# Optimization experiments

Measured on AMD Instinct MI355X. Metric: run time of the kernel, lower is better.

The kernel has to match this reference:

```python
import jax, jax.numpy as jnp
import numpy as np

H = 8          # num query heads
KV = 1         # num kv heads
D = 256        # head_dim
HID = 2048     # hidden_size
B = 4          # sequences in prefill batch
S = 2048       # tokens per sequence
T = B * S      # total tokens
NUM_SLOTS = 16384
ROPE_THETA = 10000.0


def setup_inputs() -> dict:
    key = jax.random.key(0)
    k1, k2, k3 = jax.random.split(key, 3)
    hidden_states = jax.random.normal(k1, (T, HID), dtype=jnp.float32)
    # real rotary tables: positions 0..S-1 repeated per sequence
    pos = jnp.tile(jnp.arange(S, dtype=jnp.float32), B)              # [T]
    inv_freq = 1.0 / (ROPE_THETA ** (jnp.arange(0, D, 2, dtype=jnp.float32) / D))  # [D/2]
    ang = pos[:, None] * inv_freq[None, :]                            # [T, D/2]
    cos, sin = jnp.cos(ang), jnp.sin(ang)
    slots = jnp.arange(T, dtype=jnp.int32)                            # contiguous slot mapping
    key_cache = jnp.zeros((NUM_SLOTS, KV, D), dtype=jnp.float32)
    value_cache = jnp.zeros((NUM_SLOTS, KV, D), dtype=jnp.float32)
    w_qkv = jax.random.normal(k2, ((H + 2 * KV) * D, HID), dtype=jnp.float32) * (HID ** -0.5)
    w_o = jax.random.normal(k3, (HID, H * D), dtype=jnp.float32) * ((H * D) ** -0.5)
    return {"hidden_states": hidden_states, "cos": cos, "sin": sin, "slots": slots,
            "key_cache": key_cache, "value_cache": value_cache, "w_qkv": w_qkv, "w_o": w_o}


def _rope(x, cos, sin):
    # rotate-half convention: x:[T, h, D], cos/sin:[T, D/2]
    x1, x2 = x[..., : D // 2], x[..., D // 2 :]
    c, s = cos[:, None, :], sin[:, None, :]
    return jnp.concatenate([x1 * c - x2 * s, x2 * c + x1 * s], axis=-1)


def reference(hidden_states, cos, sin, slots, key_cache, value_cache, w_qkv, w_o):
    qkv = hidden_states @ w_qkv.T                                  # [T, (H+2KV)*D]
    q = qkv[:, : H * D].reshape(T, H, D)
    k = qkv[:, H * D : (H + KV) * D].reshape(T, KV, D)
    v = qkv[:, (H + KV) * D :].reshape(T, KV, D)
    q = _rope(q, cos, sin)
    k = _rope(k, cos, sin)
    # paged_attention.reshape_and_cache: scatter post-RoPE k and raw v into cache slots
    key_cache = key_cache.at[slots].set(k)
    value_cache = value_cache.at[slots].set(v)
    # prefill flash attention: causal, per-sequence (equal-length ragged batch)
    qb = q.reshape(B, S, H, D)
    kb = jnp.repeat(k.reshape(B, S, KV, D), H // KV, axis=2)       # GQA expand
    vb = jnp.repeat(v.reshape(B, S, KV, D), H // KV, axis=2)
    scale = D ** -0.5
    scores = jnp.einsum("bqhd,bkhd->bhqk", qb, kb) * scale          # [B,H,S,S]
    causal = jnp.tril(jnp.ones((S, S), dtype=bool))
    scores = jnp.where(causal[None, None], scores, jnp.finfo(scores.dtype).min)
    probs = jax.nn.softmax(scores, axis=-1)
    attn = jnp.einsum("bhqk,bkhd->bqhd", probs, vb).reshape(T, H * D)
    out = attn @ w_o.T                                              # [T, HID]
    return out, key_cache, value_cache
```

## Files before the change

### kernel.cpp

```cpp
#include <hip/hip_runtime.h>

#define HN 8
#define DH 256
#define HID 2048
#define BB 4
#define SS 2048
#define TT (BB*SS)
#define NQKV 2560
#define NSLOTS 16384

typedef unsigned short u16;
typedef unsigned int u32;
typedef __bf16 bf16x8 __attribute__((ext_vector_type(8)));
typedef float f32x4 __attribute__((ext_vector_type(4)));
typedef u16 u16x4 __attribute__((ext_vector_type(4)));
typedef u16 u16x8 __attribute__((ext_vector_type(8)));

__device__ __forceinline__ u16 f2bf(float f) {
    u32 u = __builtin_bit_cast(u32, f);
    u = u + 0x7fffu + ((u >> 16) & 1u);
    return (u16)(u >> 16);
}
__device__ __forceinline__ float bf2f(u16 h) {
    u32 u = ((u32)h) << 16;
    return __builtin_bit_cast(float, u);
}
__device__ __forceinline__ void gload_lds16(const void* g, void* l) {
    __builtin_amdgcn_global_load_lds((__attribute__((address_space(1))) void*)g,
                                     (__attribute__((address_space(3))) void*)l,
                                     16, 0, 0);
}

__global__ __launch_bounds__(256) void cvt_f32_bf16(const float* __restrict__ in,
                                                    u16* __restrict__ out, long n) {
    long i = ((long)blockIdx.x * blockDim.x + threadIdx.x) * 4;
    long stride = (long)gridDim.x * blockDim.x * 4;
    for (; i < n; i += stride) {
        float4 v = *(const float4*)(in + i);
        u16x4 o4;
        o4[0] = f2bf(v.x); o4[1] = f2bf(v.y); o4[2] = f2bf(v.z); o4[3] = f2bf(v.w);
        *(u16x4*)(out + i) = o4;
    }
}

template<int OUTBF>
__global__ __launch_bounds__(256) void gemm_nt(const u16* __restrict__ A, const u16* __restrict__ B,
                                               void* __restrict__ C, int M, int N, int K) {
    __shared__ u16 As[128 * 32];
    __shared__ u16 Bs[128 * 32];
    const int tid = threadIdx.x;
    const int lane = tid & 63, w = tid >> 6;
    const int quad = lane >> 4, m16 = lane & 15;
    const int wm = w & 1, wn = w >> 1;
    const int r4 = tid >> 2, c8 = (tid & 3) * 8;
    const long arow = (long)blockIdx.x * 128;
    const long brow = (long)blockIdx.y * 128;

    f32x4 acc[4][4];
#pragma unroll
    for (int i = 0; i < 4; i++)
#pragma unroll
        for (int j = 0; j < 4; j++) acc[i][j] = (f32x4){0.f, 0.f, 0.f, 0.f};

    const u16* Ag = A + (arow + r4) * (long)K + c8;
    const u16* Bg = B + (brow + r4) * (long)K + c8;

    for (int k0 = 0; k0 < K; k0 += 32) {
        __syncthreads();
        gload_lds16(Ag + k0,                 (char*)As + tid * 16);
        gload_lds16(Ag + 64l * K + k0,       (char*)As + 4096 + tid * 16);
        gload_lds16(Bg + k0,                 (char*)Bs + tid * 16);
        gload_lds16(Bg + 64l * K + k0,       (char*)Bs + 4096 + tid * 16);
        __syncthreads();
        bf16x8 af[4], bfr[4];
#pragma unroll
        for (int mi = 0; mi < 4; mi++)
            af[mi] = *(const bf16x8*)(As + (wm * 64 + mi * 16 + m16) * 32 + quad * 8);
#pragma unroll
        for (int ni = 0; ni < 4; ni++)
            bfr[ni] = *(const bf16x8*)(Bs + (wn * 64 + ni * 16 + m16) * 32 + quad * 8);
#pragma unroll
        for (int mi = 0; mi < 4; mi++)
#pragma unroll
            for (int ni = 0; ni < 4; ni++)
                acc[mi][ni] = __builtin_amdgcn_mfma_f32_16x16x32_bf16(af[mi], bfr[ni], acc[mi][ni], 0, 0, 0);
    }
#pragma unroll
    for (int mi = 0; mi < 4; mi++) {
#pragma unroll
        for (int ni = 0; ni < 4; ni++) {
            long col = brow + wn * 64 + ni * 16 + m16;
#pragma unroll
            for (int r = 0; r < 4; r++) {
                long row = arow + wm * 64 + mi * 16 + quad * 4 + r;
                float v = acc[mi][ni][r];
                if (OUTBF) ((u16*)C)[row * N + col] = f2bf(v);
                else       ((float*)C)[row * N + col] = v;
            }
        }
    }
}

__global__ __launch_bounds__(256) void rope_scatter(u16* __restrict__ qkv, const float* __restrict__ cosb,
        const float* __restrict__ sinb, const int* __restrict__ slots,
        u16* __restrict__ kb, float* __restrict__ kc, float* __restrict__ vc) {
    const int t = blockIdx.x, tid = threadIdx.x;
    const long qbase = (long)t * NQKV;
#pragma unroll
    for (int i = 0; i < 4; i++) {
        int idx = tid + i * 256;
        int head = idx >> 7, d = idx & 127;
        long off = qbase + head * DH + d;
        float q1 = bf2f(qkv[off]), q2 = bf2f(qkv[off + 128]);
        float c = cosb[(long)t * 128 + d], s = sinb[(long)t * 128 + d];
        qkv[off]       = f2bf((q1 * c - q2 * s) * 0.0625f);
        qkv[off + 128] = f2bf((q2 * c + q1 * s) * 0.0625f);
    }
    const int slot = slots[t];
    if (tid < 128) {
        int d = tid;
        long off = qbase + HN * DH + d;
        float k1 = bf2f(qkv[off]), k2 = bf2f(qkv[off + 128]);
        float c = cosb[(long)t * 128 + d], s = sinb[(long)t * 128 + d];
        float kn1 = k1 * c - k2 * s, kn2 = k2 * c + k1 * s;
        kb[(long)t * DH + d]       = f2bf(kn1);
        kb[(long)t * DH + d + 128] = f2bf(kn2);
        kc[(long)slot * DH + d]       = kn1;
        kc[(long)slot * DH + d + 128] = kn2;
    }
    {
        int d = tid;
        vc[(long)slot * DH + d] = bf2f(qkv[qbase + (HN + 1) * DH + d]);
    }
}

__global__ __launch_bounds__(256) void transpose_v(const u16* __restrict__ qkv, u16* __restrict__ vbt) {
    const int tid = threadIdx.x;
    const int s0 = blockIdx.x * 64, d0 = blockIdx.y * 64, b = blockIdx.z;
#pragma unroll
    for (int i = 0; i < 2; i++) {
        int d = d0 + i * 32 + (tid >> 3);
        int s = s0 + (tid & 7) * 8;
        u16x8 v;
#pragma unroll
        for (int e = 0; e < 8; e++)
            v[e] = qkv[(long)(b * SS + s + e) * NQKV + (HN + 1) * DH + d];
        *(u16x8*)(vbt + ((long)b * DH + d) * SS + s) = v;
    }
}

__global__ __launch_bounds__(256, 3) void flash_attn(const u16* __restrict__ qkv, const u16* __restrict__ kb,
                                                     const u16* __restrict__ vbt, u16* __restrict__ attn) {
    __shared__ u16 Ks[32 * 264];
    __shared__ u16 Vt[256 * 40];
    __shared__ u16 Pl[4 * 16 * 40];
    const int tid = threadIdx.x;
    const int lane = tid & 63, w = tid >> 6;
    const int quad = lane >> 4, m16 = lane & 15;
    const int qb = (int)gridDim.x - 1 - (int)blockIdx.x;
    const int h = blockIdx.y, b = blockIdx.z;
    const int qrow_w = qb * 64 + w * 16;

    const int k_kv = tid >> 5, k_c = tid & 31;
    const int v_d = tid >> 2, v_c = tid & 3;

    bf16x8 aq[8];
    {
        const u16* qp = qkv + (long)(b * SS + qrow_w + m16) * NQKV + h * DH;
#pragma unroll
        for (int ks = 0; ks < 8; ks++)
            aq[ks] = *(const bf16x8*)(qp + ks * 32 + quad * 8);
    }
    f32x4 o[16];
#pragma unroll
    for (int i = 0; i < 16; i++) o[i] = (f32x4){0.f, 0.f, 0.f, 0.f};
    float m_run[4] = {-1e30f, -1e30f, -1e30f, -1e30f};
    float l_run[4] = {0.f, 0.f, 0.f, 0.f};
    const long kvrow0 = (long)b * SS;
    const u16* vbase = vbt + (long)b * DH * SS;
    const int ntiles = 2 * qb + 2;

    u16x8 kreg[4], vreg[4];
#pragma unroll
    for (int i = 0; i < 4; i++) {
        kreg[i] = *(const u16x8*)(kb + (kvrow0 + k_kv + i * 8) * DH + k_c * 8);
        vreg[i] = *(const u16x8*)(vbase + (long)(v_d) * SS + 0 + v_c * 8 + (long)i * 64 * SS);
    }

    for (int it = 0; it < ntiles; it++) {
        const int kv0 = it * 32;
        __syncthreads();
#pragma unroll
        for (int i = 0; i < 4; i++) {
            *(u16x8*)(Ks + (k_kv + i * 8) * 264 + k_c * 8) = kreg[i];
            *(u16x8*)(Vt + (v_d + i * 64) * 40 + v_c * 8) = vreg[i];
        }
        __syncthreads();
        if (it + 1 < ntiles) {
            const int kv1 = kv0 + 32;
#pragma unroll
            for (int i = 0; i < 4; i++) {
                kreg[i] = *(const u16x8*)(kb + (kvrow0 + kv1 + k_kv + i * 8) * DH + k_c * 8);
                vreg[i] = *(const u16x8*)(vbase + ((long)(v_d + i * 64)) * SS + kv1 + v_c * 8);
            }
        }

        f32x4 sc[2];
        sc[0] = (f32x4){0.f, 0.f, 0.f, 0.f};
        sc[1] = (f32x4){0.f, 0.f, 0.f, 0.f};
#pragma unroll
        for (int ks = 0; ks < 8; ks++)
#pragma unroll
            for (int n = 0; n < 2; n++) {
                bf16x8 kf = *(const bf16x8*)(Ks + (n * 16 + m16) * 264 + ks * 32 + quad * 8);
                sc[n] = __builtin_amdgcn_mfma_f32_16x16x32_bf16(aq[ks], kf, sc[n], 0, 0, 0);
            }
        if (it >= 2 * qb) {
            const int qg = qrow_w + quad * 4;
#pragma unroll
            for (int n = 0; n < 2; n++) {
                int kvg = kv0 + n * 16 + m16;
#pragma unroll
                for (int r = 0; r < 4; r++)
                    if (kvg > qg + r) sc[n][r] = -1e30f;
            }
        }
        float mx[4];
#pragma unroll
        for (int r = 0; r < 4; r++) mx[r] = fmaxf(sc[0][r], sc[1][r]);
        bool grow = false;
#pragma unroll
        for (int r = 0; r < 4; r++) grow = grow || (mx[r] > m_run[r] + 8.f);
        if (__any((int)grow)) {
#pragma unroll
            for (int off = 1; off <= 8; off <<= 1)
#pragma unroll
                for (int r = 0; r < 4; r++) mx[r] = fmaxf(mx[r], __shfl_xor(mx[r], off));
#pragma unroll
            for (int r = 0; r < 4; r++) {
                float mn = fmaxf(m_run[r], mx[r]);
                float alpha = __expf(m_run[r] - mn);
                m_run[r] = mn;
                l_run[r] *= alpha;
#pragma unroll
                for (int nf = 0; nf < 16; nf++) o[nf][r] *= alpha;
            }
        }
#pragma unroll
        for (int n = 0; n < 2; n++)
#pragma unroll
            for (int r = 0; r < 4; r++) {
                float p = __expf(sc[n][r] - m_run[r]);
                sc[n][r] = p;
                l_run[r] += p;
            }
#pragma unroll
        for (int n = 0; n < 2; n++)
#pragma unroll
            for (int r = 0; r < 4; r++)
                Pl[w * 640 + (quad * 4 + r) * 40 + n * 16 + m16] = f2bf(sc[n][r]);
        asm volatile("s_waitcnt lgkmcnt(0)" ::: "memory");
        __builtin_amdgcn_sched_barrier(0);
        bf16x8 ap = *(const bf16x8*)(Pl + w * 640 + m16 * 40 + quad * 8);
#pragma unroll
        for (int nf = 0; nf < 16; nf++) {
            bf16x8 vf = *(const bf16x8*)(Vt + (nf * 16 + m16) * 40 + quad * 8);
            o[nf] = __builtin_amdgcn_mfma_f32_16x16x32_bf16(ap, vf, o[nf], 0, 0, 0);
        }
    }
#pragma unroll
    for (int off = 1; off <= 8; off <<= 1)
#pragma unroll
        for (int r = 0; r < 4; r++) l_run[r] += __shfl_xor(l_run[r], off);
    float inv[4];
#pragma unroll
    for (int r = 0; r < 4; r++) inv[r] = 1.f / l_run[r];
#pragma unroll
    for (int nf = 0; nf < 16; nf++)
#pragma unroll
        for (int r = 0; r < 4; r++) {
            long row = (long)(b * SS + qrow_w + quad * 4 + r);
            attn[row * (HN * DH) + h * DH + nf * 16 + m16] = f2bf(o[nf][r] * inv[r]);
        }
}

extern "C" void kernel_launch(void* const* d_in, const int* in_sizes, int n_in,
                              void* d_out, int out_size, void* d_ws, size_t ws_size,
                              hipStream_t stream) {
    (void)in_sizes; (void)n_in; (void)out_size; (void)ws_size;
    const float* hidden = (const float*)d_in[0];
    const float* cosb   = (const float*)d_in[1];
    const float* sinb   = (const float*)d_in[2];
    const int*   slots  = (const int*)d_in[3];
    const float* kc_in  = (const float*)d_in[4];
    const float* vc_in  = (const float*)d_in[5];
    const float* w_qkv  = (const float*)d_in[6];
    const float* w_o    = (const float*)d_in[7];

    float* out    = (float*)d_out;
    float* kc_out = out + (size_t)TT * HID;
    float* vc_out = kc_out + (size_t)NSLOTS * DH;

    char* p = (char*)d_ws;
    u16* hid_b  = (u16*)p;  p += (size_t)TT * HID * 2;
    u16* wqkv_b = (u16*)p;  p += (size_t)NQKV * HID * 2;
    u16* wo_b   = (u16*)p;  p += (size_t)HID * HID * 2;
    u16* kb     = (u16*)p;  p += (size_t)TT * DH * 2;
    u16* vbt    = (u16*)p;  p += (size_t)TT * DH * 2;
    u16* attn_b = hid_b;
    u16* qkv_b  = (u16*)d_out;

    hipMemcpyAsync(kc_out, kc_in, (size_t)NSLOTS * DH * 4, hipMemcpyDeviceToDevice, stream);
    hipMemcpyAsync(vc_out, vc_in, (size_t)NSLOTS * DH * 4, hipMemcpyDeviceToDevice, stream);

    cvt_f32_bf16<<<dim3(2048), dim3(256), 0, stream>>>(hidden, hid_b, (long)TT * HID);
    cvt_f32_bf16<<<dim3(640),  dim3(256), 0, stream>>>(w_qkv, wqkv_b, (long)NQKV * HID);
    cvt_f32_bf16<<<dim3(512),  dim3(256), 0, stream>>>(w_o,   wo_b,   (long)HID * HID);

    gemm_nt<1><<<dim3(TT / 128, NQKV / 128), dim3(256), 0, stream>>>(hid_b, wqkv_b, qkv_b, TT, NQKV, HID);
    rope_scatter<<<dim3(TT), dim3(256), 0, stream>>>(qkv_b, cosb, sinb, slots, kb, kc_out, vc_out);
    transpose_v<<<dim3(SS / 64, DH / 64, BB), dim3(256), 0, stream>>>(qkv_b, vbt);
    flash_attn<<<dim3(SS / 64, HN, BB), dim3(256), 0, stream>>>(qkv_b, kb, vbt, attn_b);
    gemm_nt<0><<<dim3(TT / 128, HID / 128), dim3(256), 0, stream>>>(attn_b, wo_b, out, TT, HID, HID);
}
```

Baseline: 683.6 us.

## Load K/V tiles directly to LDS with XOR swizzle, raise occupancy, reorder q-blocks

Replaces the register-staged K/V prefetch with direct global-to-LDS loads into unpadded, XOR-swizzled shared tiles. The fragment reads are adjusted to match the swizzle. The smaller LDS footprint and freed registers allow launch bounds of 4 blocks per CU. Q-block scheduling is interleaved to balance causal work across the grid, and s_setprio is raised around the MFMA loops. The gain is lower LDS and register pressure, but the loads are now synchronous with a full vmcnt wait each tile, so the previous overlap of next-tile loads with compute is lost.

```diff
diff --git a/kernel.cpp b/kernel.cpp
--- a/kernel.cpp
+++ b/kernel.cpp
@@ -149,20 +149,23 @@
     }
 }
 
-__global__ __launch_bounds__(256, 3) void flash_attn(const u16* __restrict__ qkv, const u16* __restrict__ kb,
+__global__ __launch_bounds__(256, 4) void flash_attn(const u16* __restrict__ qkv, const u16* __restrict__ kb,
                                                      const u16* __restrict__ vbt, u16* __restrict__ attn) {
-    __shared__ u16 Ks[32 * 264];
-    __shared__ u16 Vt[256 * 40];
+    __shared__ u16 Ks[32 * 256];
+    __shared__ u16 Vt[256 * 32];
     __shared__ u16 Pl[4 * 16 * 40];
     const int tid = threadIdx.x;
     const int lane = tid & 63, w = tid >> 6;
     const int quad = lane >> 4, m16 = lane & 15;
-    const int qb = (int)gridDim.x - 1 - (int)blockIdx.x;
+    const int xr = blockIdx.x & 7, xt = blockIdx.x >> 3;
+    const int qb = (xt == 0) ? 31 - xr : (xt == 1) ? 16 + xr : (xt == 2) ? 15 - xr : xr;
     const int h = blockIdx.y, b = blockIdx.z;
     const int qrow_w = qb * 64 + w * 16;
 
-    const int k_kv = tid >> 5, k_c = tid & 31;
-    const int v_d = tid >> 2, v_c = tid & 3;
+    const int krow = tid >> 5, kg = tid & 31, kgs = kg ^ krow;
+    const int vrow = tid >> 2, vg = tid & 3,  vgs = vg ^ ((vrow >> 1) & 3);
+    const int km7 = m16 & 7;
+    const int vcol = (quad ^ ((m16 >> 1) & 3)) * 8;
 
     bf16x8 aq[8];
     {
@@ -180,42 +183,32 @@
     const u16* vbase = vbt + (long)b * DH * SS;
     const int ntiles = 2 * qb + 2;
 
-    u16x8 kreg[4], vreg[4];
-#pragma unroll
-    for (int i = 0; i < 4; i++) {
-        kreg[i] = *(const u16x8*)(kb + (kvrow0 + k_kv + i * 8) * DH + k_c * 8);
-        vreg[i] = *(const u16x8*)(vbase + (long)(v_d) * SS + 0 + v_c * 8 + (long)i * 64 * SS);
-    }
-
     for (int it = 0; it < ntiles; it++) {
         const int kv0 = it * 32;
         __syncthreads();
 #pragma unroll
         for (int i = 0; i < 4; i++) {
-            *(u16x8*)(Ks + (k_kv + i * 8) * 264 + k_c * 8) = kreg[i];
-            *(u16x8*)(Vt + (v_d + i * 64) * 40 + v_c * 8) = vreg[i];
-        }
+            gload_lds16(kb + (kvrow0 + kv0 + i * 8 + krow) * DH + kgs * 8,
+                        (char*)Ks + i * 4096 + tid * 16);
+            gload_lds16(vbase + (long)(i * 64 + vrow) * SS + kv0 + vgs * 8,
+                        (char*)Vt + i * 4096 + tid * 16);
+        }
+        asm volatile("s_waitcnt vmcnt(0)" ::: "memory");
         __syncthreads();
-        if (it + 1 < ntiles) {
-            const int kv1 = kv0 + 32;
-#pragma unroll
-            for (int i = 0; i < 4; i++) {
-                kreg[i] = *(const u16x8*)(kb + (kvrow0 + kv1 + k_kv + i * 8) * DH + k_c * 8);
-                vreg[i] = *(const u16x8*)(vbase + ((long)(v_d + i * 64)) * SS + kv1 + v_c * 8);
-            }
-        }
 
         f32x4 sc[2];
         sc[0] = (f32x4){0.f, 0.f, 0.f, 0.f};
         sc[1] = (f32x4){0.f, 0.f, 0.f, 0.f};
+        __builtin_amdgcn_s_setprio(1);
 #pragma unroll
         for (int ks = 0; ks < 8; ks++)
 #pragma unroll
             for (int n = 0; n < 2; n++) {
-                bf16x8 kf = *(const bf16x8*)(Ks + (n * 16 + m16) * 264 + ks * 32 + quad * 8);
+                bf16x8 kf = *(const bf16x8*)(Ks + (n * 16 + m16) * 256 + (((ks * 4 + quad) ^ km7) << 3));
                 sc[n] = __builtin_amdgcn_mfma_f32_16x16x32_bf16(aq[ks], kf, sc[n], 0, 0, 0);
             }
-        if (it >= 2 * qb) {
+        __builtin_amdgcn_s_setprio(0);
+        if (kv0 >= qb * 64) {
             const int qg = qrow_w + quad * 4;
 #pragma unroll
             for (int n = 0; n < 2; n++) {
@@ -262,11 +255,13 @@
         asm volatile("s_waitcnt lgkmcnt(0)" ::: "memory");
         __builtin_amdgcn_sched_barrier(0);
         bf16x8 ap = *(const bf16x8*)(Pl + w * 640 + m16 * 40 + quad * 8);
+        __builtin_amdgcn_s_setprio(1);
 #pragma unroll
         for (int nf = 0; nf < 16; nf++) {
-            bf16x8 vf = *(const bf16x8*)(Vt + (nf * 16 + m16) * 40 + quad * 8);
+            bf16x8 vf = *(const bf16x8*)(Vt + (nf * 16 + m16) * 32 + vcol);
             o[nf] = __builtin_amdgcn_mfma_f32_16x16x32_bf16(ap, vf, o[nf], 0, 0, 0);
         }
+        __builtin_amdgcn_s_setprio(0);
     }
 #pragma unroll
     for (int off = 1; off <= 8; off <<= 1)
```

After: 656.0 us. 4.0% less time.
